# Performance work log

Hardware: AMD Instinct MI355X
Metric: run time of the kernel (lower is better)

The kernel has to match this reference:

```python
import jax, jax.numpy as jnp
import numpy as np

NDIM = 3        # coordinate dimensionality
KS = 3          # kernel size per dim (odd)
DIL = 0.05      # dilation (spacing between kernel cells)
MAXD = 1.0      # max_distance cap on SDF values
G = 64          # SDF grid resolution per dim
NSDF = 8        # number of SDF grids
OUT = 32        # out_channels
K = KS ** NDIM  # 27 kernel cells
CELL = 0.031    # grid cell size -> grid extent ~2.0


def _kernel_offsets():
    r = (jnp.arange(KS, dtype=jnp.float32) - KS // 2) * DIL
    ox, oy, oz = jnp.meshgrid(r, r, r, indexing='ij')
    return jnp.stack([ox.ravel(), oy.ravel(), oz.ravel()], -1)  # [K,3]


def _rot_inv(q, v):
    # rotate v by the inverse of quaternion q (xyzw layout), broadcasting
    u = -q[..., :3]
    w = q[..., 3:4]
    c = jnp.cross(u, v)
    return v + 2.0 * jnp.cross(u, c + w * v)


def setup_inputs() -> dict:
    key = jax.random.key(0)
    ks = jax.random.split(key, 8)
    B, N, M = 2, 50000, 4
    extent = G * CELL  # ~2.0, local grid extent
    locs = jax.random.uniform(ks[0], (B, N, NDIM), jnp.float32) * extent
    idxs = jax.random.randint(ks[1], (B, M), 0, NSDF).astype(jnp.int32)
    trans = jax.random.uniform(ks[2], (B, M, NDIM), jnp.float32) * 0.2
    quat = jax.random.normal(ks[3], (B, M, 4), jnp.float32)
    quat = quat / jnp.linalg.norm(quat, axis=-1, keepdims=True)
    poses = jnp.concatenate([trans, quat], axis=-1)  # [B,M,7] = trans + quat(xyzw)
    scales = jax.random.uniform(ks[4], (B, M), jnp.float32) + 0.5
    sdf_grid = jax.random.normal(ks[5], (NSDF, G, G, G), jnp.float32) * 0.3 + 0.2
    cell_sizes = jnp.full((NSDF,), CELL, jnp.float32)
    weight = jax.random.normal(ks[6], (OUT, K), jnp.float32) * 0.1
    bias = jax.random.normal(ks[7], (OUT,), jnp.float32) * 0.1
    return dict(locs=locs, idxs=idxs, poses=poses, scales=scales,
                sdf_grid=sdf_grid, cell_sizes=cell_sizes, weight=weight, bias=bias)


def _convsdf(locs, idxs, poses, scales, sdf_grid, cell_sizes, weight, bias):
    offs = _kernel_offsets()                                  # [K,3]
    p = locs[:, :, None, :] + offs[None, None, :, :]          # [B,N,K,3] kernel-cell points
    t = poses[:, :, :NDIM]                                    # [B,M,3]
    q = poses[:, :, NDIM:]                                    # [B,M,4]
    # transform each kernel-cell point into each SDF's local frame
    r = p[:, :, :, None, :] - t[:, None, None, :, :]          # [B,N,K,M,3]
    r = _rot_inv(q[:, None, None, :, :], r)
    sc = scales[:, None, None, :, None]                       # [B,1,1,M,1]
    r = r / sc
    cs = cell_sizes[idxs][:, None, None, :, None]             # [B,1,1,M,1]
    gc = r / cs - 0.5                                         # grid coords (values at cell centers)
    inb = jnp.all((r >= 0.0) & (r <= G * cs), axis=-1)        # [B,N,K,M] inside grid?
    gcc = jnp.clip(gc, 0.0, G - 1.0)
    i0 = jnp.clip(jnp.floor(gcc), 0.0, G - 2.0).astype(jnp.int32)
    fr = gcc - i0.astype(jnp.float32)
    flat = sdf_grid.reshape(-1)
    jb = idxs.astype(jnp.int32)[:, None, None, :]             # [B,1,1,M]
    val = jnp.zeros(inb.shape, jnp.float32)
    # trilinear interpolation: 8 corner gathers
    for dx in (0, 1):
        wx = fr[..., 0] if dx else 1.0 - fr[..., 0]
        for dy in (0, 1):
            wy = fr[..., 1] if dy else 1.0 - fr[..., 1]
            for dz in (0, 1):
                wz = fr[..., 2] if dz else 1.0 - fr[..., 2]
                fi = ((jb * G + i0[..., 0] + dx) * G + i0[..., 1] + dy) * G + i0[..., 2] + dz
                val = val + wx * wy * wz * jnp.take(flat, fi)
    # scaled SDF value; out-of-grid -> max_distance, then min over objects, cap
    val = jnp.where(inb, val * sc[..., 0], MAXD)
    d = jnp.minimum(jnp.min(val, axis=-1), MAXD)              # [B,N,K]
    return jnp.einsum('bnk,ok->bno', d, weight) + bias        # [B,N,OUT]


def reference(locs, idxs, poses, scales, sdf_grid, cell_sizes, weight, bias):
    return _convsdf(locs, idxs, poses, scales, sdf_grid, cell_sizes, weight, bias)
```

## Files before the change

### kernel.cpp

```cpp
#include <hip/hip_runtime.h>
#include <hip/hip_fp16.h>
#include <math.h>

#define KK 27
#define MM 4
#define OUTC 32
#define GG 64
#define GG3 (GG * GG * GG)
#define DILF 0.05f
#define MAXDF 1.0f
#define MU 4e-3f

static __device__ inline bool exact_inb(float lx, float ly, float lz,
                                        float ox, float oy, float oz,
                                        float tx, float ty, float tz,
                                        float qx, float qy, float qz, float qw,
                                        float sc, float gcs) {
#pragma clang fp contract(off)
    float px = lx + ox, py = ly + oy, pz = lz + oz;
    float vx = px - tx, vy = py - ty, vz = pz - tz;
    float ux = -qx, uy = -qy, uz = -qz;
    float cx = uy * vz - uz * vy;
    float cy = uz * vx - ux * vz;
    float cz = ux * vy - uy * vx;
    float twx = cx + qw * vx;
    float twy = cy + qw * vy;
    float twz = cz + qw * vz;
    float rx = vx + 2.0f * (uy * twz - uz * twy);
    float ry = vy + 2.0f * (uz * twx - ux * twz);
    float rz = vz + 2.0f * (ux * twy - uy * twx);
    rx = rx / sc; ry = ry / sc; rz = rz / sc;
    return (rx >= 0.0f) & (rx <= gcs) & (ry >= 0.0f) & (ry <= gcs) &
           (rz >= 0.0f) & (rz <= gcs);
}

__global__ __launch_bounds__(256) void repack_kernel(
    const float* __restrict__ sdf, const int* __restrict__ idxs,
    unsigned int* __restrict__ zp, int nslots) {
    const int j = blockIdx.y;
    __shared__ int ref;
    if (threadIdx.x == 0) {
        int r = 0;
        for (int s = 0; s < nslots; ++s) r |= (idxs[s] == j) ? 1 : 0;
        ref = r;
    }
    __syncthreads();
    if (!ref) return;

    int i = blockIdx.x * 256 + threadIdx.x;
    int z = i & 63;
    const float* g = sdf + (size_t)j * GG3;
    float v0 = g[i];
    float v1 = g[z == 63 ? i : i + 1];
    __half2 h = __floats2half2_rn(v0, v1);
    zp[(size_t)j * GG3 + i] = *(unsigned int*)&h;
}

__global__ __launch_bounds__(256) void convsdf_zp_kernel(
    const float* __restrict__ locs, const int* __restrict__ idxs,
    const float* __restrict__ poses, const float* __restrict__ scales,
    const unsigned int* __restrict__ zp, const float* __restrict__ cells,
    const float* __restrict__ weight, const float* __restrict__ bias,
    float* __restrict__ out, int N) {
    __shared__ float4 s_ro[MM][KK];
    __shared__ float4 s_off[KK];
    __shared__ float4 s_wT4[KK * OUTC / 4];
    __shared__ float  s_bias[OUTC];
    __shared__ float  s_t[MM][3];
    __shared__ float  s_q[MM][4];
    __shared__ float  s_sc[MM];
    __shared__ float  s_gcs[MM];
    __shared__ float  s_invscs[MM];
    __shared__ int    s_goff[MM];

    const int b = blockIdx.y;
    const int tid = threadIdx.x;

    float* s_wT = (float*)s_wT4;
    for (int i = tid; i < KK * OUTC; i += 256) {
        int k = i >> 5, o = i & 31;
        s_wT[i] = weight[o * KK + k];
    }
    if (tid < OUTC) s_bias[tid] = bias[tid];
    if (tid < KK) {
        int kx = tid / 9, ky = (tid / 3) % 3, kz = tid % 3;
        s_off[tid] = make_float4((float)(kx - 1) * DILF, (float)(ky - 1) * DILF,
                                 (float)(kz - 1) * DILF, 0.0f);
    }
    if (tid >= 128 && tid < 128 + MM) {
        int m = tid - 128;
        const float* pp = poses + (b * MM + m) * 7;
        float sc = scales[b * MM + m];
        int gi = idxs[b * MM + m];
        float cs = cells[gi];
        s_t[m][0] = pp[0]; s_t[m][1] = pp[1]; s_t[m][2] = pp[2];
        s_q[m][0] = pp[3]; s_q[m][1] = pp[4]; s_q[m][2] = pp[5]; s_q[m][3] = pp[6];
        s_sc[m] = sc;
        s_gcs[m] = (float)GG * cs;
        s_invscs[m] = 1.0f / (sc * cs);
        s_goff[m] = gi * GG3;
    }
    __syncthreads();

    if (tid < MM * KK) {
        int m = tid / KK, k = tid - m * KK;
        float4 off = s_off[k];
        float qx = s_q[m][0], qy = s_q[m][1], qz = s_q[m][2], qw = s_q[m][3];
        float ux = -qx, uy = -qy, uz = -qz;
        float vx = off.x, vy = off.y, vz = off.z;
        float cx = uy * vz - uz * vy + qw * vx;
        float cy = uz * vx - ux * vz + qw * vy;
        float cz = ux * vy - uy * vx + qw * vz;
        float rx = vx + 2.0f * (uy * cz - uz * cy);
        float ry = vy + 2.0f * (uz * cx - ux * cz);
        float rz = vz + 2.0f * (ux * cy - uy * cx);
        float f = s_invscs[m];
        s_ro[m][k] = make_float4(rx * f, ry * f, rz * f, 0.0f);
    }
    __syncthreads();

    const int pl = tid >> 2;
    const int m  = tid & 3;
    const int n  = blockIdx.x * 64 + pl;
    if (n >= N) return;

    const float* lp = locs + (size_t)(b * N + n) * 3;
    float lx = lp[0], ly = lp[1], lz = lp[2];

    float tx = s_t[m][0], ty = s_t[m][1], tz = s_t[m][2];
    float qx = s_q[m][0], qy = s_q[m][1], qz = s_q[m][2], qw = s_q[m][3];
    float sc = s_sc[m], gcs = s_gcs[m];
    float bux, buy, buz;
    {
        float vx = lx - tx, vy = ly - ty, vz = lz - tz;
        float ux = -qx, uy = -qy, uz = -qz;
        float cx = uy * vz - uz * vy + qw * vx;
        float cy = uz * vx - ux * vz + qw * vy;
        float cz = ux * vy - uy * vx + qw * vz;
        float rx = vx + 2.0f * (uy * cz - uz * cy);
        float ry = vy + 2.0f * (uz * cx - ux * cz);
        float rz = vz + 2.0f * (ux * cy - uy * cx);
        float f = s_invscs[m];
        bux = rx * f; buy = ry * f; buz = rz * f;
    }
    const unsigned int* zg = zp + s_goff[m];

    float acc[8];
#pragma unroll
    for (int j = 0; j < 8; ++j) acc[j] = s_bias[m * 8 + j];

#pragma unroll 3
    for (int k = 0; k < KK; ++k) {
        float4 ro = s_ro[m][k];
        float ux = bux + ro.x;
        float uy = buy + ro.y;
        float uz = buz + ro.z;
        float mn = fminf(fminf(ux, uy), uz);
        float mx = fmaxf(fmaxf(ux, uy), uz);
        bool inb = (mn >= 0.0f) & (mx <= 64.0f);
        if ((mn > -MU) & (mx < 64.0f + MU) &
            ((mn < MU) | (mx > 64.0f - MU))) {
            float4 ofk = s_off[k];
            inb = exact_inb(lx, ly, lz, ofk.x, ofk.y, ofk.z,
                            tx, ty, tz, qx, qy, qz, qw, sc, gcs);
        }
        float v = MAXDF;
        if (inb) {
            float gx = fminf(fmaxf(ux - 0.5f, 0.0f), 63.0f);
            float gy = fminf(fmaxf(uy - 0.5f, 0.0f), 63.0f);
            float gz = fminf(fmaxf(uz - 0.5f, 0.0f), 63.0f);
            int ix = min((int)gx, 62);
            int iy = min((int)gy, 62);
            int iz = min((int)gz, 62);
            float fx = gx - (float)ix;
            float fy = gy - (float)iy;
            float fz = gz - (float)iz;
            int base = (ix * GG + iy) * GG + iz;
            unsigned int r00 = zg[base];
            unsigned int r01 = zg[base + GG];
            unsigned int r10 = zg[base + GG * GG];
            unsigned int r11 = zg[base + GG * GG + GG];
            float2 p00 = __half22float2(*(__half2*)&r00);
            float2 p01 = __half22float2(*(__half2*)&r01);
            float2 p10 = __half22float2(*(__half2*)&r10);
            float2 p11 = __half22float2(*(__half2*)&r11);
            float c00 = p00.x + fz * (p00.y - p00.x);
            float c01 = p01.x + fz * (p01.y - p01.x);
            float c10 = p10.x + fz * (p10.y - p10.x);
            float c11 = p11.x + fz * (p11.y - p11.x);
            float c0 = c00 + fy * (c01 - c00);
            float c1 = c10 + fy * (c11 - c10);
            v = (c0 + fx * (c1 - c0)) * sc;
        }
        float dk = v;
        dk = fminf(dk, __shfl_xor(dk, 1, 4));
        dk = fminf(dk, __shfl_xor(dk, 2, 4));
        float4 w0 = s_wT4[k * (OUTC / 4) + m * 2 + 0];
        float4 w1 = s_wT4[k * (OUTC / 4) + m * 2 + 1];
        acc[0] += dk * w0.x; acc[1] += dk * w0.y;
        acc[2] += dk * w0.z; acc[3] += dk * w0.w;
        acc[4] += dk * w1.x; acc[5] += dk * w1.y;
        acc[6] += dk * w1.z; acc[7] += dk * w1.w;
    }

    float* op = out + (size_t)(b * N + n) * OUTC + m * 8;
    *(float4*)&op[0] = make_float4(acc[0], acc[1], acc[2], acc[3]);
    *(float4*)&op[4] = make_float4(acc[4], acc[5], acc[6], acc[7]);
}

__global__ __launch_bounds__(256) void convsdf_direct_kernel(
    const float* __restrict__ locs, const int* __restrict__ idxs,
    const float* __restrict__ poses, const float* __restrict__ scales,
    const float* __restrict__ sdf, const float* __restrict__ cells,
    const float* __restrict__ weight, const float* __restrict__ bias,
    float* __restrict__ out, int N) {
    __shared__ float4 s_ro[MM][KK];
    __shared__ float4 s_off[KK];
    __shared__ float4 s_wT4[KK * OUTC / 4];
    __shared__ float  s_bias[OUTC];
    __shared__ float  s_t[MM][3];
    __shared__ float  s_q[MM][4];
    __shared__ float  s_sc[MM];
    __shared__ float  s_gcs[MM];
    __shared__ float  s_invscs[MM];
    __shared__ int    s_goff[MM];

    const int b = blockIdx.y;
    const int tid = threadIdx.x;

    float* s_wT = (float*)s_wT4;
    for (int i = tid; i < KK * OUTC; i += 256) {
        int k = i >> 5, o = i & 31;
        s_wT[i] = weight[o * KK + k];
    }
    if (tid < OUTC) s_bias[tid] = bias[tid];
    if (tid < KK) {
        int kx = tid / 9, ky = (tid / 3) % 3, kz = tid % 3;
        s_off[tid] = make_float4((float)(kx - 1) * DILF, (float)(ky - 1) * DILF,
                                 (float)(kz - 1) * DILF, 0.0f);
    }
    if (tid >= 128 && tid < 128 + MM) {
        int m = tid - 128;
        const float* pp = poses + (b * MM + m) * 7;
        float sc = scales[b * MM + m];
        int gi = idxs[b * MM + m];
        float cs = cells[gi];
        s_t[m][0] = pp[0]; s_t[m][1] = pp[1]; s_t[m][2] = pp[2];
        s_q[m][0] = pp[3]; s_q[m][1] = pp[4]; s_q[m][2] = pp[5]; s_q[m][3] = pp[6];
        s_sc[m] = sc;
        s_gcs[m] = (float)GG * cs;
        s_invscs[m] = 1.0f / (sc * cs);
        s_goff[m] = gi * GG3;
    }
    __syncthreads();

    if (tid < MM * KK) {
        int m = tid / KK, k = tid - m * KK;
        float4 off = s_off[k];
        float qx = s_q[m][0], qy = s_q[m][1], qz = s_q[m][2], qw = s_q[m][3];
        float ux = -qx, uy = -qy, uz = -qz;
        float vx = off.x, vy = off.y, vz = off.z;
        float cx = uy * vz - uz * vy + qw * vx;
        float cy = uz * vx - ux * vz + qw * vy;
        float cz = ux * vy - uy * vx + qw * vz;
        float rx = vx + 2.0f * (uy * cz - uz * cy);
        float ry = vy + 2.0f * (uz * cx - ux * cz);
        float rz = vz + 2.0f * (ux * cy - uy * cx);
        float f = s_invscs[m];
        s_ro[m][k] = make_float4(rx * f, ry * f, rz * f, 0.0f);
    }
    __syncthreads();

    const int pl = tid >> 2;
    const int m  = tid & 3;
    const int n  = blockIdx.x * 64 + pl;
    if (n >= N) return;

    const float* lp = locs + (size_t)(b * N + n) * 3;
    float lx = lp[0], ly = lp[1], lz = lp[2];

    float tx = s_t[m][0], ty = s_t[m][1], tz = s_t[m][2];
    float qx = s_q[m][0], qy = s_q[m][1], qz = s_q[m][2], qw = s_q[m][3];
    float sc = s_sc[m], gcs = s_gcs[m];
    float bux, buy, buz;
    {
        float vx = lx - tx, vy = ly - ty, vz = lz - tz;
        float ux = -qx, uy = -qy, uz = -qz;
        float cx = uy * vz - uz * vy + qw * vx;
        float cy = uz * vx - ux * vz + qw * vy;
        float cz = ux * vy - uy * vx + qw * vz;
        float rx = vx + 2.0f * (uy * cz - uz * cy);
        float ry = vy + 2.0f * (uz * cx - ux * cz);
        float rz = vz + 2.0f * (ux * cy - uy * cx);
        float f = s_invscs[m];
        bux = rx * f; buy = ry * f; buz = rz * f;
    }
    const float* gbase = sdf + s_goff[m];

    float acc[8];
#pragma unroll
    for (int j = 0; j < 8; ++j) acc[j] = s_bias[m * 8 + j];

#pragma unroll 3
    for (int k = 0; k < KK; ++k) {
        float4 ro = s_ro[m][k];
        float ux = bux + ro.x;
        float uy = buy + ro.y;
        float uz = buz + ro.z;
        float mn = fminf(fminf(ux, uy), uz);
        float mx = fmaxf(fmaxf(ux, uy), uz);
        bool inb = (mn >= 0.0f) & (mx <= 64.0f);
        if ((mn > -MU) & (mx < 64.0f + MU) &
            ((mn < MU) | (mx > 64.0f - MU))) {
            float4 ofk = s_off[k];
            inb = exact_inb(lx, ly, lz, ofk.x, ofk.y, ofk.z,
                            tx, ty, tz, qx, qy, qz, qw, sc, gcs);
        }
        float v = MAXDF;
        if (inb) {
            float gx = fminf(fmaxf(ux - 0.5f, 0.0f), 63.0f);
            float gy = fminf(fmaxf(uy - 0.5f, 0.0f), 63.0f);
            float gz = fminf(fmaxf(uz - 0.5f, 0.0f), 63.0f);
            int ix = min((int)gx, 62);
            int iy = min((int)gy, 62);
            int iz = min((int)gz, 62);
            float fx = gx - (float)ix;
            float fy = gy - (float)iy;
            float fz = gz - (float)iz;
            const float* g = gbase + ((ix * GG + iy) * GG + iz);
            float v000 = g[0], v001 = g[1];
            float v010 = g[GG], v011 = g[GG + 1];
            float v100 = g[GG * GG], v101 = g[GG * GG + 1];
            float v110 = g[GG * GG + GG], v111 = g[GG * GG + GG + 1];
            float c00 = v000 + fz * (v001 - v000);
            float c01 = v010 + fz * (v011 - v010);
            float c10 = v100 + fz * (v101 - v100);
            float c11 = v110 + fz * (v111 - v110);
            float c0 = c00 + fy * (c01 - c00);
            float c1 = c10 + fy * (c11 - c10);
            v = (c0 + fx * (c1 - c0)) * sc;
        }
        float dk = v;
        dk = fminf(dk, __shfl_xor(dk, 1, 4));
        dk = fminf(dk, __shfl_xor(dk, 2, 4));
        float4 w0 = s_wT4[k * (OUTC / 4) + m * 2 + 0];
        float4 w1 = s_wT4[k * (OUTC / 4) + m * 2 + 1];
        acc[0] += dk * w0.x; acc[1] += dk * w0.y;
        acc[2] += dk * w0.z; acc[3] += dk * w0.w;
        acc[4] += dk * w1.x; acc[5] += dk * w1.y;
        acc[6] += dk * w1.z; acc[7] += dk * w1.w;
    }

    float* op = out + (size_t)(b * N + n) * OUTC + m * 8;
    *(float4*)&op[0] = make_float4(acc[0], acc[1], acc[2], acc[3]);
    *(float4*)&op[4] = make_float4(acc[4], acc[5], acc[6], acc[7]);
}

extern "C" void kernel_launch(void* const* d_in, const int* in_sizes, int n_in,
                              void* d_out, int out_size, void* d_ws, size_t ws_size,
                              hipStream_t stream) {
    const float* locs   = (const float*)d_in[0];
    const int*   idxs   = (const int*)d_in[1];
    const float* poses  = (const float*)d_in[2];
    const float* scales = (const float*)d_in[3];
    const float* sdf    = (const float*)d_in[4];
    const float* cells  = (const float*)d_in[5];
    const float* weight = (const float*)d_in[6];
    const float* bias   = (const float*)d_in[7];
    float* out = (float*)d_out;

    int B = in_sizes[1] / MM;
    int N = in_sizes[0] / (3 * B);
    int NSDF = in_sizes[4] / GG3;
    int nslots = in_sizes[1];

    size_t zp_bytes = (size_t)NSDF * GG3 * 4;
    dim3 grid((N + 63) / 64, B);

    if (ws_size >= zp_bytes) {
        unsigned int* zpg = (unsigned int*)d_ws;
        dim3 gridR(GG3 / 256, NSDF);
        repack_kernel<<<gridR, 256, 0, stream>>>(sdf, idxs, zpg, nslots);
        convsdf_zp_kernel<<<grid, 256, 0, stream>>>(locs, idxs, poses, scales,
                                                    zpg, cells, weight, bias,
                                                    out, N);
    } else {
        convsdf_direct_kernel<<<grid, 256, 0, stream>>>(locs, idxs, poses,
                                                        scales, sdf, cells,
                                                        weight, bias, out, N);
    }
}
```

Measured before the change: 34.54 us.

## Pack y-neighbour pairs in half2 grid and use DPP quad min-reduce

The repacked half-precision grid now pairs each voxel with its y-neighbour instead of its z-neighbour. The trilinear gather then reads two adjacent words along z (base, base+1) per x-plane, so the loads become contiguous 8-byte accesses rather than stride-64 loads in y. The 4-lane min reduction across objects also switches from __shfl_xor to DPP quad permutes, which avoids LDS-based shuffles. The trade-off is a repack kernel that reads at a stride of GG.

Result: no change. 35.00 us (+1.3%).

```diff
diff --git a/kernel.cpp b/kernel.cpp
--- a/kernel.cpp
+++ b/kernel.cpp
@@ -34,9 +34,16 @@
            (rz >= 0.0f) & (rz <= gcs);
 }
 
+template <int CTRL>
+static __device__ inline float dpp_qperm(float x) {
+    int xi = __builtin_bit_cast(int, x);
+    int r = __builtin_amdgcn_update_dpp(xi, xi, CTRL, 0xF, 0xF, false);
+    return __builtin_bit_cast(float, r);
+}
+
 __global__ __launch_bounds__(256) void repack_kernel(
     const float* __restrict__ sdf, const int* __restrict__ idxs,
-    unsigned int* __restrict__ zp, int nslots) {
+    unsigned int* __restrict__ yp, int nslots) {
     const int j = blockIdx.y;
     __shared__ int ref;
     if (threadIdx.x == 0) {
@@ -48,18 +55,18 @@
     if (!ref) return;
 
     int i = blockIdx.x * 256 + threadIdx.x;
-    int z = i & 63;
+    int y = (i >> 6) & 63;
     const float* g = sdf + (size_t)j * GG3;
     float v0 = g[i];
-    float v1 = g[z == 63 ? i : i + 1];
+    float v1 = g[y == 63 ? i : i + GG];
     __half2 h = __floats2half2_rn(v0, v1);
-    zp[(size_t)j * GG3 + i] = *(unsigned int*)&h;
-}
-
-__global__ __launch_bounds__(256) void convsdf_zp_kernel(
+    yp[(size_t)j * GG3 + i] = *(unsigned int*)&h;
+}
+
+__global__ __launch_bounds__(256) void convsdf_yp_kernel(
     const float* __restrict__ locs, const int* __restrict__ idxs,
     const float* __restrict__ poses, const float* __restrict__ scales,
-    const unsigned int* __restrict__ zp, const float* __restrict__ cells,
+    const unsigned int* __restrict__ yp, const float* __restrict__ cells,
     const float* __restrict__ weight, const float* __restrict__ bias,
     float* __restrict__ out, int N) {
     __shared__ float4 s_ro[MM][KK];
@@ -143,7 +150,7 @@
         float f = s_invscs[m];
         bux = rx * f; buy = ry * f; buz = rz * f;
     }
-    const unsigned int* zg = zp + s_goff[m];
+    const unsigned int* qg = yp + s_goff[m];
 
     float acc[8];
 #pragma unroll
@@ -176,25 +183,25 @@
             float fy = gy - (float)iy;
             float fz = gz - (float)iz;
             int base = (ix * GG + iy) * GG + iz;
-            unsigned int r00 = zg[base];
-            unsigned int r01 = zg[base + GG];
-            unsigned int r10 = zg[base + GG * GG];
-            unsigned int r11 = zg[base + GG * GG + GG];
-            float2 p00 = __half22float2(*(__half2*)&r00);
-            float2 p01 = __half22float2(*(__half2*)&r01);
-            float2 p10 = __half22float2(*(__half2*)&r10);
-            float2 p11 = __half22float2(*(__half2*)&r11);
-            float c00 = p00.x + fz * (p00.y - p00.x);
-            float c01 = p01.x + fz * (p01.y - p01.x);
-            float c10 = p10.x + fz * (p10.y - p10.x);
-            float c11 = p11.x + fz * (p11.y - p11.x);
-            float c0 = c00 + fy * (c01 - c00);
-            float c1 = c10 + fy * (c11 - c10);
+            unsigned int a0 = qg[base];
+            unsigned int a1 = qg[base + 1];
+            unsigned int b0 = qg[base + GG * GG];
+            unsigned int b1 = qg[base + GG * GG + 1];
+            float2 pa0 = __half22float2(*(__half2*)&a0);
+            float2 pa1 = __half22float2(*(__half2*)&a1);
+            float2 pb0 = __half22float2(*(__half2*)&b0);
+            float2 pb1 = __half22float2(*(__half2*)&b1);
+            float az0 = pa0.x + fz * (pa1.x - pa0.x);
+            float az1 = pa0.y + fz * (pa1.y - pa0.y);
+            float bz0 = pb0.x + fz * (pb1.x - pb0.x);
+            float bz1 = pb0.y + fz * (pb1.y - pb0.y);
+            float c0 = az0 + fy * (az1 - az0);
+            float c1 = bz0 + fy * (bz1 - bz0);
             v = (c0 + fx * (c1 - c0)) * sc;
         }
         float dk = v;
-        dk = fminf(dk, __shfl_xor(dk, 1, 4));
-        dk = fminf(dk, __shfl_xor(dk, 2, 4));
+        dk = fminf(dk, dpp_qperm<0xB1>(dk));
+        dk = fminf(dk, dpp_qperm<0x4E>(dk));
         float4 w0 = s_wT4[k * (OUTC / 4) + m * 2 + 0];
         float4 w1 = s_wT4[k * (OUTC / 4) + m * 2 + 1];
         acc[0] += dk * w0.x; acc[1] += dk * w0.y;
@@ -341,8 +348,8 @@
             v = (c0 + fx * (c1 - c0)) * sc;
         }
         float dk = v;
-        dk = fminf(dk, __shfl_xor(dk, 1, 4));
-        dk = fminf(dk, __shfl_xor(dk, 2, 4));
+        dk = fminf(dk, dpp_qperm<0xB1>(dk));
+        dk = fminf(dk, dpp_qperm<0x4E>(dk));
         float4 w0 = s_wT4[k * (OUTC / 4) + m * 2 + 0];
         float4 w1 = s_wT4[k * (OUTC / 4) + m * 2 + 1];
         acc[0] += dk * w0.x; acc[1] += dk * w0.y;
@@ -374,15 +381,15 @@
     int NSDF = in_sizes[4] / GG3;
     int nslots = in_sizes[1];
 
-    size_t zp_bytes = (size_t)NSDF * GG3 * 4;
+    size_t yp_bytes = (size_t)NSDF * GG3 * 4;
     dim3 grid((N + 63) / 64, B);
 
-    if (ws_size >= zp_bytes) {
-        unsigned int* zpg = (unsigned int*)d_ws;
+    if (ws_size >= yp_bytes) {
+        unsigned int* ypg = (unsigned int*)d_ws;
         dim3 gridR(GG3 / 256, NSDF);
-        repack_kernel<<<gridR, 256, 0, stream>>>(sdf, idxs, zpg, nslots);
-        convsdf_zp_kernel<<<grid, 256, 0, stream>>>(locs, idxs, poses, scales,
-                                                    zpg, cells, weight, bias,
+        repack_kernel<<<gridR, 256, 0, stream>>>(sdf, idxs, ypg, nslots);
+        convsdf_yp_kernel<<<grid, 256, 0, stream>>>(locs, idxs, poses, scales,
+                                                    ypg, cells, weight, bias,
                                                     out, N);
     } else {
         convsdf_direct_kernel<<<grid, 256, 0, stream>>>(locs, idxs, poses,
```
